# Optimization experiments

Hardware: AMD Instinct MI355X
Metric: run time of the kernel (lower is better)

Reference implementation:

```python
import jax, jax.numpy as jnp
import numpy as np

N_NODES = 100000
NEG_SLOPE = 0.2  # PyG GATConv default leaky_relu slope


def _gat_conv(x, src, dst, W, a_src, a_dst, b, heads, out_c, concat):
    """One PyG-style GATConv (eval mode, dropout disabled).
    x: [N, F_in]; src/dst: [E] (src -> dst message direction, self-loops included).
    """
    N = x.shape[0]
    h = (x @ W).reshape(N, heads, out_c)                      # [N, H, C]
    alpha_s = jnp.einsum('nhc,hc->nh', h, a_src)              # [N, H]
    alpha_d = jnp.einsum('nhc,hc->nh', h, a_dst)              # [N, H]
    e = jax.nn.leaky_relu(alpha_s[src] + alpha_d[dst], NEG_SLOPE)  # [E, H]
    # segment softmax over incoming edges of each destination node
    e_max = jax.ops.segment_max(e, dst, num_segments=N)       # [N, H]
    e_exp = jnp.exp(e - e_max[dst])                           # [E, H]
    denom = jax.ops.segment_sum(e_exp, dst, num_segments=N)   # [N, H]
    alpha = e_exp / (denom[dst] + 1e-16)                      # [E, H]
    msg = h[src] * alpha[:, :, None]                          # [E, H, C]
    out = jax.ops.segment_sum(msg, dst, num_segments=N)       # [N, H, C]
    out = out.reshape(N, heads * out_c) if concat else out.mean(axis=1)
    return out + b


def setup_inputs() -> dict:
    key = jax.random.key(0)
    ks = jax.random.split(key, 16)
    N, E, F_in = N_NODES, 400000, 128
    H = 4
    h1, h2, out_dim = 128, 64, 2

    def glorot(k, shape, fan_in):
        return jax.random.normal(k, shape, dtype=jnp.float32) * (1.0 / np.sqrt(fan_in))

    inp = {
        'x': jax.random.normal(ks[0], (N, F_in), dtype=jnp.float32),
        'edge_index': jax.random.randint(ks[1], (2, E), 0, N, dtype=jnp.int64),
        'W1': glorot(ks[2], (F_in, H * h1), F_in),
        'a_src1': glorot(ks[3], (H, h1), h1),
        'a_dst1': glorot(ks[4], (H, h1), h1),
        'b1': jnp.zeros((H * h1,), dtype=jnp.float32),
        'W2': glorot(ks[5], (H * h1, H * h2), H * h1),
        'a_src2': glorot(ks[6], (H, h2), h2),
        'a_dst2': glorot(ks[7], (H, h2), h2),
        'b2': jnp.zeros((H * h2,), dtype=jnp.float32),
        # layer 3: 256 -> 2, heads=1, concat=False (mean)
        'W3': glorot(ks[8], (H * h2, 1 * out_dim), H * h2),
        'a_src3': glorot(ks[9], (1, out_dim), out_dim),
        'a_dst3': glorot(ks[10], (1, out_dim), out_dim),
        'b3': jnp.zeros((out_dim,), dtype=jnp.float32),
    }
    return inp


def reference(x, edge_index, W1, a_src1, a_dst1, b1, W2, a_src2, a_dst2, b2,
              W3, a_src3, a_dst3, b3):
    N = x.shape[0]
    # add self-loops (PyG GATConv default add_self_loops=True)
    loop = jnp.arange(N, dtype=edge_index.dtype)
    src = jnp.concatenate([edge_index[0], loop])
    dst = jnp.concatenate([edge_index[1], loop])

    h = _gat_conv(x, src, dst, W1, a_src1, a_dst1, b1, heads=4, out_c=128, concat=True)
    h = jax.nn.elu(h)  # dropout is identity in eval mode
    h = _gat_conv(h, src, dst, W2, a_src2, a_dst2, b2, heads=4, out_c=64, concat=True)
    h = jax.nn.elu(h)
    out = _gat_conv(h, src, dst, W3, a_src3, a_dst3, b3, heads=1, out_c=2, concat=False)
    return out
```

## Files before the change

kernel.cpp:

```cpp
#include <hip/hip_runtime.h>
#include <hip/hip_bf16.h>
#include <math.h>


#define LEAKY_SLOPE 0.2f

typedef __attribute__((ext_vector_type(8))) short bf16x8;
typedef __attribute__((ext_vector_type(4))) float f32x4;
typedef __attribute__((ext_vector_type(4))) float fx4;

__device__ __forceinline__ unsigned short f2bf(float f) {
    unsigned int x = __float_as_uint(f);
    x += 0x7fffu + ((x >> 16) & 1u);
    return (unsigned short)(x >> 16);
}
__device__ __forceinline__ float bf2f(unsigned short u) {
    return __uint_as_float(((unsigned int)u) << 16);
}
__device__ __forceinline__ float elu(float x) {
    return (x > 0.f) ? x : (__expf(x) - 1.f);
}

__device__ __forceinline__ void gll16(const void* g, void* l) {
    __builtin_amdgcn_global_load_lds((const __attribute__((address_space(1))) void*)g,
                                     (__attribute__((address_space(3))) void*)l, 16, 0, 0);
}

__device__ __forceinline__ int edge_val(const int* __restrict__ ei, int is64, long long idx) {
    return is64 ? ei[2 * idx] : ei[idx];
}

__global__ void detect_kernel(const unsigned int* __restrict__ ei, int* __restrict__ flag) {
    int lane = threadIdx.x;
    unsigned int v = ei[2 * lane + 1];
    unsigned long long b = __ballot(v != 0u);
    if (lane == 0) *flag = (b == 0ull) ? 1 : 0;
}

__global__ __launch_bounds__(256) void zero2_kernel(int* __restrict__ a, int* __restrict__ b, int n) {
    int i = blockIdx.x * blockDim.x + threadIdx.x;
    if (i < n) { a[i] = 0; b[i] = 0; }
}

__global__ __launch_bounds__(256) void sentinel_kernel(float* __restrict__ out, int n, float v) {
    int i = blockIdx.x * blockDim.x + threadIdx.x;
    if (i < n) out[i] = v;
}

__global__ __launch_bounds__(256) void count_kernel(const int* __restrict__ ei,
                                                    const int* __restrict__ flag,
                                                    int E, int N, int* __restrict__ counts) {
    int e = blockIdx.x * blockDim.x + threadIdx.x;
    if (e >= E + N) return;
    int is64 = *flag;
    int d = (e < E) ? edge_val(ei, is64, (long long)E + e) : (e - E);
    atomicAdd(&counts[d], 1);
}

__global__ __launch_bounds__(256) void scan_block_kernel(const int* __restrict__ counts,
                                                         int* __restrict__ ptrArr,
                                                         int* __restrict__ bsums, int N) {
    __shared__ int sh[256];
    int t = threadIdx.x, i = blockIdx.x * 256 + t;
    int v = (i < N) ? counts[i] : 0;
    sh[t] = v;
    __syncthreads();
    for (int off = 1; off < 256; off <<= 1) {
        int u = (t >= off) ? sh[t - off] : 0;
        __syncthreads();
        sh[t] += u;
        __syncthreads();
    }
    if (i < N) ptrArr[i] = sh[t] - v;
    if (t == 255) bsums[blockIdx.x] = sh[255];
}

__global__ __launch_bounds__(1024) void scan_tops_kernel(const int* __restrict__ bsums,
                                                         int* __restrict__ boff, int nb,
                                                         int* __restrict__ totalOut) {
    __shared__ int sh[1024];
    int t = threadIdx.x;
    int v = (t < nb) ? bsums[t] : 0;
    sh[t] = v;
    __syncthreads();
    for (int off = 1; off < 1024; off <<= 1) {
        int u = (t >= off) ? sh[t - off] : 0;
        __syncthreads();
        sh[t] += u;
        __syncthreads();
    }
    if (t < nb) boff[t] = sh[t] - v;
    if (t == 1023) *totalOut = sh[1023];
}

__global__ __launch_bounds__(256) void scan_add_kernel(int* __restrict__ ptrArr,
                                                       const int* __restrict__ boff, int N) {
    int i = blockIdx.x * blockDim.x + threadIdx.x;
    if (i < N) ptrArr[i] += boff[i >> 8];
}

__global__ __launch_bounds__(256) void fill_kernel(const int* __restrict__ ei,
                                                   const int* __restrict__ flag,
                                                   int E, int N,
                                                   const int* __restrict__ ptrArr,
                                                   int* __restrict__ cursor,
                                                   int* __restrict__ csr_src) {
    int e = blockIdx.x * blockDim.x + threadIdx.x;
    if (e >= E + N) return;
    int is64 = *flag;
    int s, d;
    if (e < E) {
        s = edge_val(ei, is64, e);
        d = edge_val(ei, is64, (long long)E + e);
    } else {
        s = d = e - E;
    }
    int slot = atomicAdd(&cursor[d], 1);
    csr_src[ptrArr[d] + slot] = s;
}

__global__ __launch_bounds__(256) void transpose_w_kernel(const float* __restrict__ W,
                                                          unsigned short* __restrict__ Wt,
                                                          int K, int Nn) {
    int i = blockIdx.x * blockDim.x + threadIdx.x;
    if (i >= K * Nn) return;
    int n = i / K, k = i - n * K;
    Wt[i] = f2bf(W[(size_t)k * Nn + n]);
}

__global__ __launch_bounds__(256) void proj_attn_kernel(const float* __restrict__ W1,
                                                        const float* __restrict__ a_s,
                                                        const float* __restrict__ a_d,
                                                        float* __restrict__ ws1,
                                                        float* __restrict__ wd1) {
    int t = blockIdx.x * blockDim.x + threadIdx.x;
    if (t >= 1024) return;
    int k = t >> 3, sd = (t >> 2) & 1, h = t & 3;
    const float* a = sd ? a_d : a_s;
    float s = 0.f;
    const float* wr = W1 + (size_t)k * 512 + h * 128;
    const float* ar = a + h * 128;
    for (int c = 0; c < 128; ++c) s += wr[c] * ar[c];
    (sd ? wd1 : ws1)[k * 4 + h] = s;
}

__global__ __launch_bounds__(256) void alpha_x_kernel(const float* __restrict__ x,
                                                      const float* __restrict__ ws1,
                                                      const float* __restrict__ wd1,
                                                      float* __restrict__ out_s,
                                                      float* __restrict__ out_d,
                                                      unsigned short* __restrict__ xbf, int N) {
    int lane = threadIdx.x & 63;
    int wid = threadIdx.x >> 6;
    int n = blockIdx.x * (blockDim.x >> 6) + wid;
    if (n >= N) return;
    int k0 = lane * 2;
    float2 xv = *(const float2*)(x + (size_t)n * 128 + k0);
    alignas(4) unsigned short o[2] = {f2bf(xv.x), f2bf(xv.y)};
    *(unsigned int*)(xbf + (size_t)n * 128 + k0) = *(unsigned int*)o;
    fx4 s0 = *(const fx4*)(ws1 + k0 * 4);
    fx4 s1 = *(const fx4*)(ws1 + k0 * 4 + 4);
    fx4 d0 = *(const fx4*)(wd1 + k0 * 4);
    fx4 d1 = *(const fx4*)(wd1 + k0 * 4 + 4);
    float ps[4], pd[4];
#pragma unroll
    for (int h = 0; h < 4; ++h) {
        ps[h] = xv.x * s0[h] + xv.y * s1[h];
        pd[h] = xv.x * d0[h] + xv.y * d1[h];
    }
#pragma unroll
    for (int off = 32; off; off >>= 1)
#pragma unroll
        for (int h = 0; h < 4; ++h) {
            ps[h] += __shfl_xor(ps[h], off);
            pd[h] += __shfl_xor(pd[h], off);
        }
    if (lane == 0) {
        fx4 rs = {ps[0], ps[1], ps[2], ps[3]};
        fx4 rd = {pd[0], pd[1], pd[2], pd[3]};
        *(fx4*)(out_s + (size_t)n * 4) = rs;
        *(fx4*)(out_d + (size_t)n * 4) = rd;
    }
}

__global__ __launch_bounds__(256) void sm_aggx_kernel(const int* __restrict__ ptrArr,
                                                      const int* __restrict__ csr_src,
                                                      const float* __restrict__ as,
                                                      const float* __restrict__ ad,
                                                      const unsigned short* __restrict__ xbf,
                                                      unsigned short* __restrict__ aggX, int N) {
    __shared__ float sal[4][64][4];
    int lane = threadIdx.x & 63;
    int wid = threadIdx.x >> 6;
    int n = blockIdx.x * 4 + wid;
    if (n >= N) return;
    int beg = ptrArr[n], end = ptrArr[n + 1];
    int deg = end - beg;
    fx4 dv = *(const fx4*)(ad + (size_t)n * 4);
    float acc[4][2];
#pragma unroll
    for (int h = 0; h < 4; ++h) { acc[h][0] = 0.f; acc[h][1] = 0.f; }

    if (deg <= 64) {
        bool act = lane < deg;
        int i = beg + (act ? lane : 0);
        int s = csr_src[i];
        fx4 av = *(const fx4*)(as + (size_t)s * 4);
        float e[4];
#pragma unroll
        for (int h = 0; h < 4; ++h) {
            float xx = av[h] + dv[h];
            xx = (xx >= 0.f) ? xx : LEAKY_SLOPE * xx;
            e[h] = act ? xx : -INFINITY;
        }
#pragma unroll
        for (int h = 0; h < 4; ++h) {
            float mm = e[h];
#pragma unroll
            for (int off = 32; off; off >>= 1) mm = fmaxf(mm, __shfl_xor(mm, off));
            float ex = __expf(e[h] - mm);
            float ss = ex;
#pragma unroll
            for (int off = 32; off; off >>= 1) ss += __shfl_xor(ss, off);
            sal[wid][lane][h] = ex / (ss + 1e-16f);
        }
        for (int i2 = beg; i2 < end; i2 += 4) {
            int r = end - i2;
            int e1 = (r > 1) ? i2 + 1 : i2;
            int e2 = (r > 2) ? i2 + 2 : i2;
            int e3 = (r > 3) ? i2 + 3 : i2;
            int s0 = csr_src[i2], s1 = csr_src[e1], s2 = csr_src[e2], s3 = csr_src[e3];
            fx4 a0 = *(const fx4*)&sal[wid][i2 - beg][0];
            fx4 a1 = *(const fx4*)&sal[wid][e1 - beg][0];
            fx4 a2 = *(const fx4*)&sal[wid][e2 - beg][0];
            fx4 a3 = *(const fx4*)&sal[wid][e3 - beg][0];
            if (r <= 1) a1 = (fx4){0.f, 0.f, 0.f, 0.f};
            if (r <= 2) a2 = (fx4){0.f, 0.f, 0.f, 0.f};
            if (r <= 3) a3 = (fx4){0.f, 0.f, 0.f, 0.f};
            unsigned int r0 = *(const unsigned int*)(xbf + (size_t)s0 * 128 + lane * 2);
            unsigned int r1 = *(const unsigned int*)(xbf + (size_t)s1 * 128 + lane * 2);
            unsigned int r2 = *(const unsigned int*)(xbf + (size_t)s2 * 128 + lane * 2);
            unsigned int r3 = *(const unsigned int*)(xbf + (size_t)s3 * 128 + lane * 2);
            float x00 = bf2f((unsigned short)r0), x01 = bf2f((unsigned short)(r0 >> 16));
            float x10 = bf2f((unsigned short)r1), x11 = bf2f((unsigned short)(r1 >> 16));
            float x20 = bf2f((unsigned short)r2), x21 = bf2f((unsigned short)(r2 >> 16));
            float x30 = bf2f((unsigned short)r3), x31 = bf2f((unsigned short)(r3 >> 16));
#pragma unroll
            for (int h = 0; h < 4; ++h) {
                acc[h][0] += a0[h] * x00 + a1[h] * x10 + a2[h] * x20 + a3[h] * x30;
                acc[h][1] += a0[h] * x01 + a1[h] * x11 + a2[h] * x21 + a3[h] * x31;
            }
        }
    } else {
        float m[4], inv[4];
#pragma unroll
        for (int h = 0; h < 4; ++h) m[h] = -INFINITY;
        for (int i = beg + lane; i < end; i += 64) {
            int s = csr_src[i];
            fx4 av = *(const fx4*)(as + (size_t)s * 4);
#pragma unroll
            for (int h = 0; h < 4; ++h) {
                float v = av[h] + dv[h];
                v = (v >= 0.f) ? v : LEAKY_SLOPE * v;
                m[h] = fmaxf(m[h], v);
            }
        }
#pragma unroll
        for (int h = 0; h < 4; ++h)
#pragma unroll
            for (int off = 32; off; off >>= 1) m[h] = fmaxf(m[h], __shfl_xor(m[h], off));
        float ss[4] = {0.f, 0.f, 0.f, 0.f};
        for (int i = beg + lane; i < end; i += 64) {
            int s = csr_src[i];
            fx4 av = *(const fx4*)(as + (size_t)s * 4);
#pragma unroll
            for (int h = 0; h < 4; ++h) {
                float v = av[h] + dv[h];
                v = (v >= 0.f) ? v : LEAKY_SLOPE * v;
                ss[h] += __expf(v - m[h]);
            }
        }
#pragma unroll
        for (int h = 0; h < 4; ++h) {
#pragma unroll
            for (int off = 32; off; off >>= 1) ss[h] += __shfl_xor(ss[h], off);
            inv[h] = 1.f / (ss[h] + 1e-16f);
        }
        for (int i = beg; i < end; ++i) {
            int s = csr_src[i];
            fx4 av = *(const fx4*)(as + (size_t)s * 4);
            unsigned int rr = *(const unsigned int*)(xbf + (size_t)s * 128 + lane * 2);
            float x0 = bf2f((unsigned short)rr), x1 = bf2f((unsigned short)(rr >> 16));
#pragma unroll
            for (int h = 0; h < 4; ++h) {
                float v = av[h] + dv[h];
                v = (v >= 0.f) ? v : LEAKY_SLOPE * v;
                float al = __expf(v - m[h]) * inv[h];
                acc[h][0] += al * x0;
                acc[h][1] += al * x1;
            }
        }
    }
#pragma unroll
    for (int h = 0; h < 4; ++h) {
        alignas(4) unsigned short o[2] = {f2bf(acc[h][0]), f2bf(acc[h][1])};
        *(unsigned int*)(aggX + (size_t)h * N * 128 + (size_t)n * 128 + lane * 2) = *(unsigned int*)o;
    }
}

template <int K, int KCHUNK, int C_HEAD, bool BIAS_ELU>
__global__ __launch_bounds__(256) void gemm_kernel(const unsigned short* __restrict__ A,
                                                   int lda, long long a_plane,
                                                   const unsigned short* __restrict__ Bt,
                                                   unsigned short* __restrict__ C,
                                                   const float* __restrict__ a_src,
                                                   const float* __restrict__ a_dst,
                                                   float* __restrict__ alpha_s,
                                                   float* __restrict__ alpha_d,
                                                   const float* __restrict__ bias,
                                                   int M, int N) {
    constexpr int CPR = KCHUNK / 8;
    constexpr int ITS = 128 * CPR / 256;
    __shared__ unsigned short As[128 * KCHUNK];
    const int bm = blockIdx.y, bn = blockIdx.x;
    const int tid = threadIdx.x;
    const int lane = tid & 63, wid = tid >> 6;
    const int wr = wid >> 1, wc = wid & 1;
    const int l15 = lane & 15, l4 = lane >> 4;
    const unsigned short* Ab = A + (size_t)bn * a_plane;
    f32x4 acc[4][4];
#pragma unroll
    for (int m = 0; m < 4; ++m)
#pragma unroll
        for (int n = 0; n < 4; ++n) acc[m][n] = (f32x4){0.f, 0.f, 0.f, 0.f};

    for (int kc = 0; kc < K / KCHUNK; ++kc) {
        if (kc) __syncthreads();
#pragma unroll
        for (int it = 0; it < ITS; ++it) {
            int idx = it * 256 + tid;
            int row = idx / CPR;
            int ch = idx % CPR;
            int src = ch ^ (row & 7);
            int grow = bm * 128 + row;
            const unsigned short* g = Ab + (size_t)grow * lda + kc * KCHUNK + src * 8;
            char* l = (char*)As + it * 4096 + wid * 1024;
            if (grow < M) gll16(g, l);
        }
        __syncthreads();
#pragma unroll
        for (int step = 0; step < KCHUNK / 32; ++step) {
            bf16x8 af[4], bfr[4];
            int kb = step * 64 + l4 * 16;
#pragma unroll
            for (int m = 0; m < 4; ++m) {
                int r = wr * 64 + m * 16 + l15;
                af[m] = *(const bf16x8*)((const char*)As + r * (2 * KCHUNK) + (kb ^ ((r & 7) << 4)));
            }
#pragma unroll
            for (int n = 0; n < 4; ++n) {
                int rB = bn * 128 + wc * 64 + n * 16 + l15;
                bfr[n] = *(const bf16x8*)(Bt + (size_t)rB * K + kc * KCHUNK + step * 32 + l4 * 8);
            }
#pragma unroll
            for (int m = 0; m < 4; ++m)
#pragma unroll
                for (int n = 0; n < 4; ++n)
                    acc[m][n] = __builtin_amdgcn_mfma_f32_16x16x32_bf16(bfr[n], af[m], acc[m][n], 0, 0, 0);
        }
    }
#pragma unroll
    for (int m = 0; m < 4; ++m) {
        int row = bm * 128 + wr * 64 + m * 16 + l15;
        if (row < M) {
#pragma unroll
            for (int n = 0; n < 4; ++n) {
                int col = bn * 128 + wc * 64 + n * 16 + l4 * 4;
                f32x4 v = acc[m][n];
                if (BIAS_ELU) {
                    fx4 bb = *(const fx4*)(bias + col);
#pragma unroll
                    for (int j = 0; j < 4; ++j) v[j] = elu(v[j] + bb[j]);
                }
                alignas(8) unsigned short o[4] = {f2bf(v[0]), f2bf(v[1]), f2bf(v[2]), f2bf(v[3])};
                *(uint2*)(C + (size_t)row * N + col) = *(uint2*)o;
            }
        }
    }
    if constexpr (C_HEAD == 64) {
        const int H = N / C_HEAD;
        float ps[4], pd[4];
#pragma unroll
        for (int m = 0; m < 4; ++m) { ps[m] = 0.f; pd[m] = 0.f; }
#pragma unroll
        for (int n = 0; n < 4; ++n) {
            int col = bn * 128 + wc * 64 + n * 16 + l4 * 4;
            fx4 asv = *(const fx4*)(a_src + col);
            fx4 adv = *(const fx4*)(a_dst + col);
#pragma unroll
            for (int m = 0; m < 4; ++m)
#pragma unroll
                for (int j = 0; j < 4; ++j) {
                    ps[m] += acc[m][n][j] * asv[j];
                    pd[m] += acc[m][n][j] * adv[j];
                }
        }
#pragma unroll
        for (int m = 0; m < 4; ++m) {
            ps[m] += __shfl_xor(ps[m], 16); ps[m] += __shfl_xor(ps[m], 32);
            pd[m] += __shfl_xor(pd[m], 16); pd[m] += __shfl_xor(pd[m], 32);
        }
        if (lane < 16) {
            int head = bn * 2 + wc;
#pragma unroll
            for (int m = 0; m < 4; ++m) {
                int row = bm * 128 + wr * 64 + m * 16 + l15;
                if (row < M) {
                    alpha_s[(size_t)row * H + head] = ps[m];
                    alpha_d[(size_t)row * H + head] = pd[m];
                }
            }
        }
    }
}

__global__ __launch_bounds__(256) void sm_agg2_kernel(const int* __restrict__ ptrArr,
                                                      const int* __restrict__ csr_src,
                                                      const float* __restrict__ as,
                                                      const float* __restrict__ ad,
                                                      const unsigned short* __restrict__ hmat,
                                                      const float* __restrict__ bias,
                                                      unsigned short* __restrict__ out, int N) {
    __shared__ float sal[4][64][4];
    int lane = threadIdx.x & 63;
    int wid = threadIdx.x >> 6;
    int n = blockIdx.x * 4 + wid;
    if (n >= N) return;
    int beg = ptrArr[n], end = ptrArr[n + 1];
    int deg = end - beg;
    int head = lane >> 4;
    fx4 dv = *(const fx4*)(ad + (size_t)n * 4);
    float acc[4] = {0.f, 0.f, 0.f, 0.f};

    if (deg <= 64) {
        bool act = lane < deg;
        int i = beg + (act ? lane : 0);
        int s = csr_src[i];
        fx4 av = *(const fx4*)(as + (size_t)s * 4);
        float e[4];
#pragma unroll
        for (int h = 0; h < 4; ++h) {
            float xx = av[h] + dv[h];
            xx = (xx >= 0.f) ? xx : LEAKY_SLOPE * xx;
            e[h] = act ? xx : -INFINITY;
        }
#pragma unroll
        for (int h = 0; h < 4; ++h) {
            float mm = e[h];
#pragma unroll
            for (int off = 32; off; off >>= 1) mm = fmaxf(mm, __shfl_xor(mm, off));
            float ex = __expf(e[h] - mm);
            float ss = ex;
#pragma unroll
            for (int off = 32; off; off >>= 1) ss += __shfl_xor(ss, off);
            sal[wid][lane][h] = ex / (ss + 1e-16f);
        }
        for (int i2 = beg; i2 < end; i2 += 4) {
            int r = end - i2;
            int e1 = (r > 1) ? i2 + 1 : i2;
            int e2 = (r > 2) ? i2 + 2 : i2;
            int e3 = (r > 3) ? i2 + 3 : i2;
            int s0 = csr_src[i2], s1 = csr_src[e1], s2 = csr_src[e2], s3 = csr_src[e3];
            float al0 = sal[wid][i2 - beg][head];
            float al1 = (r > 1) ? sal[wid][e1 - beg][head] : 0.f;
            float al2 = (r > 2) ? sal[wid][e2 - beg][head] : 0.f;
            float al3 = (r > 3) ? sal[wid][e3 - beg][head] : 0.f;
            alignas(8) unsigned short v0[4], v1[4], v2[4], v3[4];
            *(uint2*)v0 = *(const uint2*)(hmat + (size_t)s0 * 256 + lane * 4);
            *(uint2*)v1 = *(const uint2*)(hmat + (size_t)s1 * 256 + lane * 4);
            *(uint2*)v2 = *(const uint2*)(hmat + (size_t)s2 * 256 + lane * 4);
            *(uint2*)v3 = *(const uint2*)(hmat + (size_t)s3 * 256 + lane * 4);
#pragma unroll
            for (int t = 0; t < 4; ++t)
                acc[t] += al0 * bf2f(v0[t]) + al1 * bf2f(v1[t]) + al2 * bf2f(v2[t]) + al3 * bf2f(v3[t]);
        }
    } else {
        float m[4], inv[4];
#pragma unroll
        for (int h = 0; h < 4; ++h) m[h] = -INFINITY;
        for (int i = beg + lane; i < end; i += 64) {
            int s = csr_src[i];
            fx4 av = *(const fx4*)(as + (size_t)s * 4);
#pragma unroll
            for (int h = 0; h < 4; ++h) {
                float v = av[h] + dv[h];
                v = (v >= 0.f) ? v : LEAKY_SLOPE * v;
                m[h] = fmaxf(m[h], v);
            }
        }
#pragma unroll
        for (int h = 0; h < 4; ++h)
#pragma unroll
            for (int off = 32; off; off >>= 1) m[h] = fmaxf(m[h], __shfl_xor(m[h], off));
        float ss[4] = {0.f, 0.f, 0.f, 0.f};
        for (int i = beg + lane; i < end; i += 64) {
            int s = csr_src[i];
            fx4 av = *(const fx4*)(as + (size_t)s * 4);
#pragma unroll
            for (int h = 0; h < 4; ++h) {
                float v = av[h] + dv[h];
                v = (v >= 0.f) ? v : LEAKY_SLOPE * v;
                ss[h] += __expf(v - m[h]);
            }
        }
#pragma unroll
        for (int h = 0; h < 4; ++h) {
#pragma unroll
            for (int off = 32; off; off >>= 1) ss[h] += __shfl_xor(ss[h], off);
            inv[h] = 1.f / (ss[h] + 1e-16f);
        }
        float mh = m[head], invh = inv[head];
        float adh = dv[head];
        for (int i = beg; i < end; ++i) {
            int s = csr_src[i];
            float v = as[(size_t)s * 4 + head] + adh;
            v = (v >= 0.f) ? v : LEAKY_SLOPE * v;
            float al = __expf(v - mh) * invh;
            alignas(8) unsigned short vv[4];
            *(uint2*)vv = *(const uint2*)(hmat + (size_t)s * 256 + lane * 4);
#pragma unroll
            for (int t = 0; t < 4; ++t) acc[t] += al * bf2f(vv[t]);
        }
    }
    alignas(8) unsigned short o[4];
#pragma unroll
    for (int t = 0; t < 4; ++t) o[t] = f2bf(elu(acc[t] + bias[lane * 4 + t]));
    *(uint2*)(out + (size_t)n * 256 + lane * 4) = *(uint2*)o;
}

__global__ __launch_bounds__(256) void layer3_gemm_kernel(const unsigned short* __restrict__ x,
                                                          const float* __restrict__ W,
                                                          const float* __restrict__ a_s,
                                                          const float* __restrict__ a_d,
                                                          float* __restrict__ h3,
                                                          float* __restrict__ out_s,
                                                          float* __restrict__ out_d, int N) {
    int lane = threadIdx.x & 63;
    int wid = threadIdx.x >> 6;
    int n = blockIdx.x * (blockDim.x >> 6) + wid;
    if (n >= N) return;
    const unsigned short* xr = x + (size_t)n * 256 + lane * 4;
    alignas(8) unsigned short v[4];
    *(uint2*)v = *(const uint2*)xr;
    int k0 = lane * 4;
    fx4 w0 = *(const fx4*)(W + k0 * 2);
    fx4 w1 = *(const fx4*)(W + k0 * 2 + 4);
    float a0 = bf2f(v[0]) * w0[0] + bf2f(v[1]) * w0[2] + bf2f(v[2]) * w1[0] + bf2f(v[3]) * w1[2];
    float a1 = bf2f(v[0]) * w0[1] + bf2f(v[1]) * w0[3] + bf2f(v[2]) * w1[1] + bf2f(v[3]) * w1[3];
#pragma unroll
    for (int off = 32; off; off >>= 1) {
        a0 += __shfl_xor(a0, off);
        a1 += __shfl_xor(a1, off);
    }
    if (lane == 0) {
        h3[(size_t)n * 2 + 0] = a0;
        h3[(size_t)n * 2 + 1] = a1;
        out_s[n] = a0 * a_s[0] + a1 * a_s[1];
        out_d[n] = a0 * a_d[0] + a1 * a_d[1];
    }
}

__global__ __launch_bounds__(256) void sm_agg3_kernel(const int* __restrict__ ptrArr,
                                                      const int* __restrict__ csr_src,
                                                      const float* __restrict__ as,
                                                      const float* __restrict__ ad,
                                                      const float* __restrict__ h3,
                                                      const float* __restrict__ b3,
                                                      float* __restrict__ out, int N) {
    int lane = threadIdx.x & 63;
    int wid = threadIdx.x >> 6;
    int n = blockIdx.x * 4 + wid;
    if (n >= N) return;
    int beg = ptrArr[n], end = ptrArr[n + 1];
    int deg = end - beg;
    float adv = ad[n];
    float p0 = 0.f, p1 = 0.f;
    if (deg <= 64) {
        bool act = lane < deg;
        int i = beg + (act ? lane : 0);
        int s = csr_src[i];
        float xx = as[s] + adv;
        xx = (xx >= 0.f) ? xx : LEAKY_SLOPE * xx;
        float e = act ? xx : -INFINITY;
        float mm = e;
#pragma unroll
        for (int off = 32; off; off >>= 1) mm = fmaxf(mm, __shfl_xor(mm, off));
        float ex = __expf(e - mm);
        float ss = ex;
#pragma unroll
        for (int off = 32; off; off >>= 1) ss += __shfl_xor(ss, off);
        float al = ex / (ss + 1e-16f);
        float2 hv = act ? *(const float2*)(h3 + (size_t)s * 2) : make_float2(0.f, 0.f);
        p0 = al * hv.x;
        p1 = al * hv.y;
#pragma unroll
        for (int off = 32; off; off >>= 1) {
            p0 += __shfl_xor(p0, off);
            p1 += __shfl_xor(p1, off);
        }
    } else {
        float m = -INFINITY;
        for (int i = beg + lane; i < end; i += 64) {
            int s = csr_src[i];
            float v = as[s] + adv;
            v = (v >= 0.f) ? v : LEAKY_SLOPE * v;
            m = fmaxf(m, v);
        }
#pragma unroll
        for (int off = 32; off; off >>= 1) m = fmaxf(m, __shfl_xor(m, off));
        float ss = 0.f;
        for (int i = beg + lane; i < end; i += 64) {
            int s = csr_src[i];
            float v = as[s] + adv;
            v = (v >= 0.f) ? v : LEAKY_SLOPE * v;
            ss += __expf(v - m);
        }
#pragma unroll
        for (int off = 32; off; off >>= 1) ss += __shfl_xor(ss, off);
        float inv = 1.f / (ss + 1e-16f);
        for (int i = beg + lane; i < end; i += 64) {
            int s = csr_src[i];
            float v = as[s] + adv;
            v = (v >= 0.f) ? v : LEAKY_SLOPE * v;
            float al = __expf(v - m) * inv;
            float2 hv = *(const float2*)(h3 + (size_t)s * 2);
            p0 += al * hv.x;
            p1 += al * hv.y;
        }
#pragma unroll
        for (int off = 32; off; off >>= 1) {
            p0 += __shfl_xor(p0, off);
            p1 += __shfl_xor(p1, off);
        }
    }
    if (lane == 0) {
        out[(size_t)n * 2 + 0] = p0 + b3[0];
        out[(size_t)n * 2 + 1] = p1 + b3[1];
    }
}


extern "C" void kernel_launch(void* const* d_in, const int* in_sizes, int n_in,
                              void* d_out, int out_size, void* d_ws, size_t ws_size,
                              hipStream_t stream) {
    const float* x      = (const float*)d_in[0];
    const int*   ei     = (const int*)d_in[1];
    const float* W1     = (const float*)d_in[2];
    const float* a_src1 = (const float*)d_in[3];
    const float* a_dst1 = (const float*)d_in[4];
    const float* b1     = (const float*)d_in[5];
    const float* W2     = (const float*)d_in[6];
    const float* a_src2 = (const float*)d_in[7];
    const float* a_dst2 = (const float*)d_in[8];
    const float* b2     = (const float*)d_in[9];
    const float* W3     = (const float*)d_in[10];
    const float* a_src3 = (const float*)d_in[11];
    const float* a_dst3 = (const float*)d_in[12];
    const float* b3     = (const float*)d_in[13];

    const int N = in_sizes[0] / 128;
    const int E = in_sizes[1] / 2;
    const int ET = E + N;
    const int nb = (N + 255) / 256;

    size_t need = 0;
    auto carve = [&](size_t bytes) -> size_t {
        size_t off = need;
        need += (bytes + 255) & ~(size_t)255;
        return off;
    };
    size_t o_counts   = carve((size_t)N * 4);
    size_t o_cursor   = carve((size_t)N * 4);
    size_t o_ptr      = carve((size_t)(N + 1) * 4);
    size_t o_csr      = carve((size_t)ET * 4);
    size_t o_flag     = carve(4);
    size_t o_bsums    = carve((size_t)2048 * 4);
    size_t o_boff     = carve((size_t)2048 * 4);
    size_t o_alpha_s  = carve((size_t)N * 4 * 4);
    size_t o_alpha_d  = carve((size_t)N * 4 * 4);
    size_t o_h3       = carve((size_t)N * 2 * 4);
    size_t o_wsd      = carve((size_t)128 * 4 * 4 * 2);
    size_t o_wt1      = carve((size_t)512 * 128 * 2);
    size_t o_wt2      = carve((size_t)256 * 512 * 2);
    size_t o_xbf      = carve((size_t)N * 128 * 2);
    size_t o_bufA     = carve((size_t)N * 512 * 2);
    size_t o_bufB     = carve((size_t)N * 512 * 2);

    if (need > ws_size) {
        sentinel_kernel<<<(out_size + 255) / 256, 256, 0, stream>>>(
            (float*)d_out, out_size, (float)(ws_size >> 20));
        return;
    }

    char* w = (char*)d_ws;
    int*   counts   = (int*)(w + o_counts);
    int*   cursor   = (int*)(w + o_cursor);
    int*   ptrArr   = (int*)(w + o_ptr);
    int*   csr_src  = (int*)(w + o_csr);
    int*   flag     = (int*)(w + o_flag);
    int*   bsums    = (int*)(w + o_bsums);
    int*   boff     = (int*)(w + o_boff);
    float* alpha_s  = (float*)(w + o_alpha_s);
    float* alpha_d  = (float*)(w + o_alpha_d);
    float* h3       = (float*)(w + o_h3);
    float* ws1      = (float*)(w + o_wsd);
    float* wd1      = ws1 + 128 * 4;
    unsigned short* Wt1  = (unsigned short*)(w + o_wt1);
    unsigned short* Wt2  = (unsigned short*)(w + o_wt2);
    unsigned short* xbf  = (unsigned short*)(w + o_xbf);
    unsigned short* bufA = (unsigned short*)(w + o_bufA);
    unsigned short* bufB = (unsigned short*)(w + o_bufB);

    const int edge_blocks = (ET + 255) / 256;
    const int node_wave_blocks = (N + 3) / 4;
    const int node_thr_blocks = (N + 255) / 256;

    zero2_kernel<<<node_thr_blocks, 256, 0, stream>>>(counts, cursor, N);
    detect_kernel<<<1, 64, 0, stream>>>((const unsigned int*)ei, flag);
    count_kernel<<<edge_blocks, 256, 0, stream>>>(ei, flag, E, N, counts);
    scan_block_kernel<<<nb, 256, 0, stream>>>(counts, ptrArr, bsums, N);
    scan_tops_kernel<<<1, 1024, 0, stream>>>(bsums, boff, nb, ptrArr + N);
    scan_add_kernel<<<node_thr_blocks, 256, 0, stream>>>(ptrArr, boff, N);
    fill_kernel<<<edge_blocks, 256, 0, stream>>>(ei, flag, E, N, ptrArr, cursor, csr_src);

    transpose_w_kernel<<<(512 * 128 + 255) / 256, 256, 0, stream>>>(W1, Wt1, 128, 512);
    transpose_w_kernel<<<(256 * 512 + 255) / 256, 256, 0, stream>>>(W2, Wt2, 512, 256);
    proj_attn_kernel<<<4, 256, 0, stream>>>(W1, a_src1, a_dst1, ws1, wd1);

    {
        alpha_x_kernel<<<node_wave_blocks, 256, 0, stream>>>(x, ws1, wd1, alpha_s, alpha_d, xbf, N);
        sm_aggx_kernel<<<node_wave_blocks, 256, 0, stream>>>(ptrArr, csr_src, alpha_s, alpha_d, xbf, bufA, N);
        dim3 g(4, (N + 127) / 128);
        gemm_kernel<128, 128, 0, true><<<g, 256, 0, stream>>>(
            bufA, 128, (long long)N * 128, Wt1, bufB,
            nullptr, nullptr, nullptr, nullptr, b1, N, 512);
    }
    {
        dim3 g(2, (N + 127) / 128);
        gemm_kernel<512, 128, 64, false><<<g, 256, 0, stream>>>(
            bufB, 512, 0LL, Wt2, bufA,
            a_src2, a_dst2, alpha_s, alpha_d, nullptr, N, 256);
        sm_agg2_kernel<<<node_wave_blocks, 256, 0, stream>>>(ptrArr, csr_src, alpha_s, alpha_d, bufA, b2, bufB, N);
    }
    {
        layer3_gemm_kernel<<<node_wave_blocks, 256, 0, stream>>>(bufB, W3, a_src3, a_dst3, h3, alpha_s, alpha_d, N);
        sm_agg3_kernel<<<node_wave_blocks, 256, 0, stream>>>(ptrArr, csr_src, alpha_s, alpha_d, h3, b3, (float*)d_out, N);
    }
}
```

Baseline: 450.1 us.

## Fuse layer-1 and layer-2 GEMMs keeping h1 tile in shared memory

Replaces the two separate GEMM launches (aggregated-x times W1 with bias+ELU, then h1 times W2 with attention projections) with one kernel per 64-row tile. Each block builds the 64x512 bf16 h1 tile in swizzled LDS and immediately multiplies it by W2, so the 512-wide h1 matrix is never written to or read back from global memory. The cost is a large LDS footprint per block (about 128 KB), which limits occupancy, and fewer rows per block.

```diff
diff --git a/kernel.cpp b/kernel.cpp
--- a/kernel.cpp
+++ b/kernel.cpp
@@ -308,59 +308,58 @@
     }
 }
 
-template <int K, int KCHUNK, int C_HEAD, bool BIAS_ELU>
-__global__ __launch_bounds__(256) void gemm_kernel(const unsigned short* __restrict__ A,
-                                                   int lda, long long a_plane,
-                                                   const unsigned short* __restrict__ Bt,
-                                                   unsigned short* __restrict__ C,
-                                                   const float* __restrict__ a_src,
-                                                   const float* __restrict__ a_dst,
-                                                   float* __restrict__ alpha_s,
-                                                   float* __restrict__ alpha_d,
-                                                   const float* __restrict__ bias,
-                                                   int M, int N) {
-    constexpr int CPR = KCHUNK / 8;
-    constexpr int ITS = 128 * CPR / 256;
-    __shared__ unsigned short As[128 * KCHUNK];
-    const int bm = blockIdx.y, bn = blockIdx.x;
+__global__ __launch_bounds__(256) void fused12_kernel(const unsigned short* __restrict__ aggX,
+                                                      const unsigned short* __restrict__ Wt1,
+                                                      const unsigned short* __restrict__ Wt2,
+                                                      const float* __restrict__ b1,
+                                                      const float* __restrict__ a_src2,
+                                                      const float* __restrict__ a_dst2,
+                                                      unsigned short* __restrict__ h2,
+                                                      float* __restrict__ alpha_s,
+                                                      float* __restrict__ alpha_d,
+                                                      int M) {
+    __shared__ unsigned short h1[64 * 512];
+    __shared__ unsigned short stg[4 * 64 * 128];
+    const int bm = blockIdx.x;
     const int tid = threadIdx.x;
     const int lane = tid & 63, wid = tid >> 6;
-    const int wr = wid >> 1, wc = wid & 1;
     const int l15 = lane & 15, l4 = lane >> 4;
-    const unsigned short* Ab = A + (size_t)bn * a_plane;
+
+    const unsigned short* plane = aggX + (size_t)wid * M * 128;
+    {
+        char* base = (char*)stg + wid * 16384;
+#pragma unroll
+        for (int it = 0; it < 16; ++it) {
+            int idx = it * 64 + lane;
+            int row = idx >> 4, ch = idx & 15;
+            int src = ch ^ (row & 7);
+            int grow = bm * 64 + row;
+            if (grow < M) gll16(plane + (size_t)grow * 128 + src * 8, base + it * 1024);
+        }
+    }
+    __syncthreads();
+
+    const char* Asw = (const char*)stg + wid * 16384;
     f32x4 acc[4][4];
-#pragma unroll
-    for (int m = 0; m < 4; ++m)
-#pragma unroll
-        for (int n = 0; n < 4; ++n) acc[m][n] = (f32x4){0.f, 0.f, 0.f, 0.f};
-
-    for (int kc = 0; kc < K / KCHUNK; ++kc) {
-        if (kc) __syncthreads();
-#pragma unroll
-        for (int it = 0; it < ITS; ++it) {
-            int idx = it * 256 + tid;
-            int row = idx / CPR;
-            int ch = idx % CPR;
-            int src = ch ^ (row & 7);
-            int grow = bm * 128 + row;
-            const unsigned short* g = Ab + (size_t)grow * lda + kc * KCHUNK + src * 8;
-            char* l = (char*)As + it * 4096 + wid * 1024;
-            if (grow < M) gll16(g, l);
-        }
-        __syncthreads();
-#pragma unroll
-        for (int step = 0; step < KCHUNK / 32; ++step) {
+
+    for (int half = 0; half < 2; ++half) {
+#pragma unroll
+        for (int m = 0; m < 4; ++m)
+#pragma unroll
+            for (int n = 0; n < 4; ++n) acc[m][n] = (f32x4){0.f, 0.f, 0.f, 0.f};
+#pragma unroll
+        for (int step = 0; step < 4; ++step) {
             bf16x8 af[4], bfr[4];
             int kb = step * 64 + l4 * 16;
 #pragma unroll
             for (int m = 0; m < 4; ++m) {
-                int r = wr * 64 + m * 16 + l15;
-                af[m] = *(const bf16x8*)((const char*)As + r * (2 * KCHUNK) + (kb ^ ((r & 7) << 4)));
+                int rl = m * 16 + l15;
+                af[m] = *(const bf16x8*)(Asw + rl * 256 + (kb ^ ((rl & 7) << 4)));
             }
 #pragma unroll
             for (int n = 0; n < 4; ++n) {
-                int rB = bn * 128 + wc * 64 + n * 16 + l15;
-                bfr[n] = *(const bf16x8*)(Bt + (size_t)rB * K + kc * KCHUNK + step * 32 + l4 * 8);
+                int rB = wid * 128 + half * 64 + n * 16 + l15;
+                bfr[n] = *(const bf16x8*)(Wt1 + (size_t)rB * 128 + step * 32 + l4 * 8);
             }
 #pragma unroll
             for (int m = 0; m < 4; ++m)
@@ -368,57 +367,88 @@
                 for (int n = 0; n < 4; ++n)
                     acc[m][n] = __builtin_amdgcn_mfma_f32_16x16x32_bf16(bfr[n], af[m], acc[m][n], 0, 0, 0);
         }
+#pragma unroll
+        for (int m = 0; m < 4; ++m) {
+            int rl = m * 16 + l15;
+#pragma unroll
+            for (int n = 0; n < 4; ++n) {
+                int col = wid * 128 + half * 64 + n * 16 + l4 * 4;
+                fx4 bb = *(const fx4*)(b1 + col);
+                f32x4 v = acc[m][n];
+                alignas(8) unsigned short o[4];
+#pragma unroll
+                for (int j = 0; j < 4; ++j) o[j] = f2bf(elu(v[j] + bb[j]));
+                int byteoff = (col * 2) ^ ((rl & 7) << 4);
+                *(uint2*)((char*)h1 + rl * 1024 + byteoff) = *(uint2*)o;
+            }
+        }
+    }
+    __syncthreads();
+
+#pragma unroll
+    for (int m = 0; m < 4; ++m)
+#pragma unroll
+        for (int n = 0; n < 4; ++n) acc[m][n] = (f32x4){0.f, 0.f, 0.f, 0.f};
+    for (int step = 0; step < 16; ++step) {
+        bf16x8 af[4], bfr[4];
+        int kb = step * 64 + l4 * 16;
+#pragma unroll
+        for (int m = 0; m < 4; ++m) {
+            int rl = m * 16 + l15;
+            af[m] = *(const bf16x8*)((const char*)h1 + rl * 1024 + (kb ^ ((rl & 7) << 4)));
+        }
+#pragma unroll
+        for (int n = 0; n < 4; ++n) {
+            int rB = wid * 64 + n * 16 + l15;
+            bfr[n] = *(const bf16x8*)(Wt2 + (size_t)rB * 512 + step * 32 + l4 * 8);
+        }
+#pragma unroll
+        for (int m = 0; m < 4; ++m)
+#pragma unroll
+            for (int n = 0; n < 4; ++n)
+                acc[m][n] = __builtin_amdgcn_mfma_f32_16x16x32_bf16(bfr[n], af[m], acc[m][n], 0, 0, 0);
     }
 #pragma unroll
     for (int m = 0; m < 4; ++m) {
-        int row = bm * 128 + wr * 64 + m * 16 + l15;
+        int row = bm * 64 + m * 16 + l15;
         if (row < M) {
 #pragma unroll
             for (int n = 0; n < 4; ++n) {
-                int col = bn * 128 + wc * 64 + n * 16 + l4 * 4;
+                int col = wid * 64 + n * 16 + l4 * 4;
                 f32x4 v = acc[m][n];
-                if (BIAS_ELU) {
-                    fx4 bb = *(const fx4*)(bias + col);
-#pragma unroll
-                    for (int j = 0; j < 4; ++j) v[j] = elu(v[j] + bb[j]);
-                }
                 alignas(8) unsigned short o[4] = {f2bf(v[0]), f2bf(v[1]), f2bf(v[2]), f2bf(v[3])};
-                *(uint2*)(C + (size_t)row * N + col) = *(uint2*)o;
-            }
-        }
-    }
-    if constexpr (C_HEAD == 64) {
-        const int H = N / C_HEAD;
-        float ps[4], pd[4];
-#pragma unroll
-        for (int m = 0; m < 4; ++m) { ps[m] = 0.f; pd[m] = 0.f; }
-#pragma unroll
-        for (int n = 0; n < 4; ++n) {
-            int col = bn * 128 + wc * 64 + n * 16 + l4 * 4;
-            fx4 asv = *(const fx4*)(a_src + col);
-            fx4 adv = *(const fx4*)(a_dst + col);
-#pragma unroll
-            for (int m = 0; m < 4; ++m)
-#pragma unroll
-                for (int j = 0; j < 4; ++j) {
-                    ps[m] += acc[m][n][j] * asv[j];
-                    pd[m] += acc[m][n][j] * adv[j];
-                }
-        }
+                *(uint2*)(h2 + (size_t)row * 256 + col) = *(uint2*)o;
+            }
+        }
+    }
+    float ps[4], pd[4];
+#pragma unroll
+    for (int m = 0; m < 4; ++m) { ps[m] = 0.f; pd[m] = 0.f; }
+#pragma unroll
+    for (int n = 0; n < 4; ++n) {
+        int col = wid * 64 + n * 16 + l4 * 4;
+        fx4 asv = *(const fx4*)(a_src2 + col);
+        fx4 adv = *(const fx4*)(a_dst2 + col);
+#pragma unroll
+        for (int m = 0; m < 4; ++m)
+#pragma unroll
+            for (int j = 0; j < 4; ++j) {
+                ps[m] += acc[m][n][j] * asv[j];
+                pd[m] += acc[m][n][j] * adv[j];
+            }
+    }
+#pragma unroll
+    for (int m = 0; m < 4; ++m) {
+        ps[m] += __shfl_xor(ps[m], 16); ps[m] += __shfl_xor(ps[m], 32);
+        pd[m] += __shfl_xor(pd[m], 16); pd[m] += __shfl_xor(pd[m], 32);
+    }
+    if (lane < 16) {
 #pragma unroll
         for (int m = 0; m < 4; ++m) {
-            ps[m] += __shfl_xor(ps[m], 16); ps[m] += __shfl_xor(ps[m], 32);
-            pd[m] += __shfl_xor(pd[m], 16); pd[m] += __shfl_xor(pd[m], 32);
-        }
-        if (lane < 16) {
-            int head = bn * 2 + wc;
-#pragma unroll
-            for (int m = 0; m < 4; ++m) {
-                int row = bm * 128 + wr * 64 + m * 16 + l15;
-                if (row < M) {
-                    alpha_s[(size_t)row * H + head] = ps[m];
-                    alpha_d[(size_t)row * H + head] = pd[m];
-                }
+            int row = bm * 64 + m * 16 + l15;
+            if (row < M) {
+                alpha_s[(size_t)row * 4 + wid] = ps[m];
+                alpha_d[(size_t)row * 4 + wid] = pd[m];
             }
         }
     }
@@ -737,23 +767,15 @@
     transpose_w_kernel<<<(256 * 512 + 255) / 256, 256, 0, stream>>>(W2, Wt2, 512, 256);
     proj_attn_kernel<<<4, 256, 0, stream>>>(W1, a_src1, a_dst1, ws1, wd1);
 
-    {
-        alpha_x_kernel<<<node_wave_blocks, 256, 0, stream>>>(x, ws1, wd1, alpha_s, alpha_d, xbf, N);
-        sm_aggx_kernel<<<node_wave_blocks, 256, 0, stream>>>(ptrArr, csr_src, alpha_s, alpha_d, xbf, bufA, N);
-        dim3 g(4, (N + 127) / 128);
-        gemm_kernel<128, 128, 0, true><<<g, 256, 0, stream>>>(
-            bufA, 128, (long long)N * 128, Wt1, bufB,
-            nullptr, nullptr, nullptr, nullptr, b1, N, 512);
-    }
-    {
-        dim3 g(2, (N + 127) / 128);
-        gemm_kernel<512, 128, 64, false><<<g, 256, 0, stream>>>(
-            bufB, 512, 0LL, Wt2, bufA,
-            a_src2, a_dst2, alpha_s, alpha_d, nullptr, N, 256);
-        sm_agg2_kernel<<<node_wave_blocks, 256, 0, stream>>>(ptrArr, csr_src, alpha_s, alpha_d, bufA, b2, bufB, N);
-    }
-    {
-        layer3_gemm_kernel<<<node_wave_blocks, 256, 0, stream>>>(bufB, W3, a_src3, a_dst3, h3, alpha_s, alpha_d, N);
-        sm_agg3_kernel<<<node_wave_blocks, 256, 0, stream>>>(ptrArr, csr_src, alpha_s, alpha_d, h3, b3, (float*)d_out, N);
-    }
-}
+    alpha_x_kernel<<<node_wave_blocks, 256, 0, stream>>>(x, ws1, wd1, alpha_s, alpha_d, xbf, N);
+    sm_aggx_kernel<<<node_wave_blocks, 256, 0, stream>>>(ptrArr, csr_src, alpha_s, alpha_d, xbf, bufA, N);
+
+    fused12_kernel<<<(N + 63) / 64, 256, 0, stream>>>(bufA, Wt1, Wt2, b1,
+                                                      a_src2, a_dst2, bufB,
+                                                      alpha_s, alpha_d, N);
+
+    sm_agg2_kernel<<<node_wave_blocks, 256, 0, stream>>>(ptrArr, csr_src, alpha_s, alpha_d, bufB, b2, bufA, N);
+
+    layer3_gemm_kernel<<<node_wave_blocks, 256, 0, stream>>>(bufA, W3, a_src3, a_dst3, h3, alpha_s, alpha_d, N);
+    sm_agg3_kernel<<<node_wave_blocks, 256, 0, stream>>>(ptrArr, csr_src, alpha_s, alpha_d, h3, b3, (float*)d_out, N);
+}
```

Measured after the change: 442.0 us. About the same (-1.8%).
